# Kernel optimization log

Hardware: AMD Instinct MI355X
Metric: run time of the kernel (lower is better)

Reference implementation:

```python
import jax, jax.numpy as jnp
import numpy as np

B = 512            # graphs in batch
N = 246            # ROIs per graph per node type (Brainnetome atlas)
D = 256            # node feature dim (in_channels)
DEG = 32           # edges per node per edge type
RATIO = 0.8
K = int(np.ceil(RATIO * N))   # 197 nodes kept per graph (PyG topk uses ceil)
NT = B * N                    # total nodes per node type
E = B * N * DEG               # total edges per edge type
SLOPE = 0.2                   # HANConv leaky_relu negative slope


def _seg_softmax(logits, seg, num_segments):
    # numerically stable softmax over edges grouped by destination node
    m = jax.ops.segment_max(logits, seg, num_segments=num_segments)
    m = jnp.where(jnp.isfinite(m), m, 0.0)
    e = jnp.exp(logits - m[seg])
    s = jax.ops.segment_sum(e, seg, num_segments=num_segments)
    return e / (s[seg] + 1e-16)


def _edge_type_out(h_src, h_dst, ei, a_src, a_dst, n_dst):
    # one HANConv metapath: GAT-style attention + sum-aggregate + relu
    row, col = ei[0], ei[1]
    logit = jax.nn.leaky_relu((h_src * a_src).sum(-1)[row] + (h_dst * a_dst).sum(-1)[col], SLOPE)
    alpha = _seg_softmax(logit, col, n_dst)
    out = jax.ops.segment_sum(h_src[row] * alpha[:, None], col, num_segments=n_dst)
    return jax.nn.relu(out)


def _group(o1, o2, k_w, k_b, q):
    # HANConv semantic attention over the 2 metapaths hitting a node type
    stk = jnp.stack([o1, o2])                    # [2, NT, 1]
    t = jnp.tanh(stk @ k_w + k_b).mean(axis=1)   # [2, 1]
    w = jax.nn.softmax((q * t).sum(-1))          # [2]
    return (w[:, None, None] * stk).sum(0)       # [NT, 1]


def _han_scores(x_bold, x_dti, pw_b, pb_b, pw_d, pb_d, att, k_w, k_b, q, ei_bb, ei_bd, ei_db, ei_dd):
    h_b = x_bold @ pw_b + pb_b   # [NT, 1]
    h_d = x_dti @ pw_d + pb_d
    o_bb = _edge_type_out(h_b, h_b, ei_bb, att[0, 0], att[0, 1], NT)  # dst bold
    o_bd = _edge_type_out(h_b, h_d, ei_bd, att[1, 0], att[1, 1], NT)  # dst dti
    o_db = _edge_type_out(h_d, h_b, ei_db, att[2, 0], att[2, 1], NT)  # dst bold
    o_dd = _edge_type_out(h_d, h_d, ei_dd, att[3, 0], att[3, 1], NT)  # dst dti
    s_bold = _group(o_bb, o_db, k_w, k_b, q)[:, 0]
    s_dti = _group(o_bd, o_dd, k_w, k_b, q)[:, 0]
    return s_bold, s_dti


def _topk(score):
    # per-graph top-K (all graphs have exactly N nodes -> static K)
    _, idx = jax.lax.top_k(score.reshape(B, N), K)
    return (idx + (jnp.arange(B, dtype=idx.dtype) * N)[:, None]).reshape(-1)


def _mask_of(perm, num_nodes):
    return jnp.full((num_nodes,), -1, dtype=jnp.int32).at[perm].set(
        jnp.arange(perm.shape[0], dtype=jnp.int32))


def _filter(ei, mask_row, mask_col):
    # jit-compatible variant of filter_adj: keep full edge length, mark
    # dropped edges with -1 and return the validity mask (no compaction).
    r, c = mask_row[ei[0]], mask_col[ei[1]]
    valid = (r >= 0) & (c >= 0)
    return jnp.stack([jnp.where(valid, r, -1), jnp.where(valid, c, -1)]), valid


def setup_inputs() -> dict:
    key = jax.random.key(0)
    ks = jax.random.split(key, 12)

    def edges(k):
        k1, k2 = jax.random.split(k)
        base = jnp.repeat(jnp.arange(B, dtype=jnp.int32) * N, N * DEG)
        row = base + jax.random.randint(k1, (E,), 0, N, dtype=jnp.int32)
        col = base + jax.random.randint(k2, (E,), 0, N, dtype=jnp.int32)
        return jnp.stack([row, col])

    batch = jnp.repeat(jnp.arange(B, dtype=jnp.int32), N)
    return {
        "x_bold": jax.random.normal(ks[0], (NT, D), jnp.float32),
        "x_dti": jax.random.normal(ks[1], (NT, D), jnp.float32),
        "proj_w_bold": jax.random.normal(ks[2], (D, 1), jnp.float32) / np.float32(np.sqrt(D)),
        "proj_b_bold": jnp.zeros((1,), jnp.float32),
        "proj_w_dti": jax.random.normal(ks[3], (D, 1), jnp.float32) / np.float32(np.sqrt(D)),
        "proj_b_dti": jnp.zeros((1,), jnp.float32),
        "att": jax.random.normal(ks[4], (4, 2, 1), jnp.float32),
        "k_lin_w": jax.random.normal(ks[5], (1, 1), jnp.float32),
        "k_lin_b": jnp.zeros((1,), jnp.float32),
        "q": jax.random.normal(ks[6], (1,), jnp.float32),
        "ei_bb": edges(ks[7]),
        "ei_bd": edges(ks[8]),
        "ei_db": edges(ks[9]),
        "ei_dd": edges(ks[10]),
        "batch_bold": batch,
        "batch_dti": batch,
    }


def reference(x_bold, x_dti, proj_w_bold, proj_b_bold, proj_w_dti, proj_b_dti,
              att, k_lin_w, k_lin_b, q, ei_bb, ei_bd, ei_db, ei_dd,
              batch_bold, batch_dti):
    s_bold, s_dti = _han_scores(x_bold, x_dti, proj_w_bold, proj_b_bold,
                                proj_w_dti, proj_b_dti, att, k_lin_w, k_lin_b, q,
                                ei_bb, ei_bd, ei_db, ei_dd)
    perm_b = _topk(s_bold)
    perm_d = _topk(s_dti)
    xb = x_bold[perm_b] * jnp.tanh(s_bold[perm_b])[:, None]
    xd = x_dti[perm_d] * jnp.tanh(s_dti[perm_d])[:, None]
    mb = _mask_of(perm_b, NT)
    md = _mask_of(perm_d, NT)
    bb_f, v_bb = _filter(ei_bb, mb, mb)   # filter_adj_single on bold-bold
    dd_f, v_dd = _filter(ei_dd, md, md)   # filter_adj_single on dti-dti
    bd_f, v_bd = _filter(ei_bd, mb, md)   # filter_adj_multi mode=1
    db_f, v_db = _filter(ei_db, md, mb)   # filter_adj_multi mode=2
    return (xb, xd, bb_f, v_bb, bd_f, v_bd, db_f, v_db, dd_f, v_dd,
            batch_bold[perm_b], batch_dti[perm_d], perm_b, perm_d, s_bold, s_dti)
```

## Files before the change

kernel.cpp:

```cpp
#include <hip/hip_runtime.h>
#include <cmath>

#define BB   512
#define NN   246
#define DD   256
#define DEGC 32
#define KK   197
#define NTOT (BB*NN)
#define EE   (BB*NN*DEGC)
#define EPG  (NN*DEGC)
#define EPG4 (EPG/4)
#define BKK  (BB*KK)

#define O_XB     0LL
#define O_XD     25821184LL
#define O_E0     51642368LL
#define STRIDE3E 12091392LL
#define O_BATCHB 100007936LL
#define O_BATCHD 100108800LL
#define O_PERMB  100209664LL
#define O_PERMD  100310528LL
#define O_SB     100411392LL
#define O_SD     100537344LL

typedef float vf4 __attribute__((ext_vector_type(4)));
typedef int   vi4 __attribute__((ext_vector_type(4)));

__device__ __forceinline__ vi4 nt_load_i4(const int* p) {
    return __builtin_nontemporal_load((const vi4*)p);
}
__device__ __forceinline__ vf4 nt_load_f4(const float* p) {
    return __builtin_nontemporal_load((const vf4*)p);
}
__device__ __forceinline__ void nt_store_f4(float* p, vf4 v) {
    __builtin_nontemporal_store(v, (vf4*)p);
}
__device__ __forceinline__ void nt_store_f(float* p, float v) {
    __builtin_nontemporal_store(v, p);
}

__global__ __launch_bounds__(256) void proj_kernel(
    const float* __restrict__ xb, const float* __restrict__ xd,
    const float* __restrict__ wb, const float* __restrict__ bbp,
    const float* __restrict__ wd, const float* __restrict__ bdp,
    float* __restrict__ hb, float* __restrict__ hd,
    double* __restrict__ sums) {
    if (blockIdx.x == 0 && threadIdx.x < 4) sums[threadIdx.x] = 0.0;
    int wid  = (blockIdx.x * 256 + threadIdx.x) >> 6;
    int lane = threadIdx.x & 63;
    if (wid >= 2 * NTOT) return;
    const float* x; const float* w; const float* bp; float* h; int node;
    if (wid < NTOT) { x = xb; w = wb; bp = bbp; h = hb; node = wid; }
    else            { x = xd; w = wd; bp = bdp; h = hd; node = wid - NTOT; }
    vf4 xv = nt_load_f4(x + (long long)node * DD + 4 * lane);
    vf4 wv = *(const vf4*)(w + 4 * lane);
    double acc = (double)xv.x * wv.x + (double)xv.y * wv.y +
                 (double)xv.z * wv.z + (double)xv.w * wv.w;
#pragma unroll
    for (int m = 32; m; m >>= 1) acc += __shfl_xor(acc, m, 64);
    if (lane == 0) h[node] = __fadd_rn((float)acc, bp[0]);
}

__global__ __launch_bounds__(512) void att_kernel(
    const int* __restrict__ ei_bb, const int* __restrict__ ei_bd,
    const int* __restrict__ ei_db, const int* __restrict__ ei_dd,
    const float* __restrict__ hb, const float* __restrict__ hd,
    const float* __restrict__ att, const float* __restrict__ kwp,
    const float* __restrict__ kbp, float* __restrict__ o,
    double* __restrict__ sums) {
    __shared__ float hs_sh[NN];
    __shared__ float hd_sh[NN];
    __shared__ float s_sh[NN];
    __shared__ float num_sh[NN];
    __shared__ double part[8];

    int bid = blockIdx.x;
    int t   = bid >> 9;
    int g   = bid & 511;
    const int* ei = (t == 0) ? ei_bb : (t == 1) ? ei_bd : (t == 2) ? ei_db : ei_dd;
    const float* hs  = (t >= 2) ? hd : hb;
    const float* hdt = (t & 1)  ? hd : hb;
    float a_src = att[2 * t], a_dst = att[2 * t + 1];
    int base = g * NN;
    int tid  = threadIdx.x;

    if (tid < NN) {
        hs_sh[tid]  = hs[base + tid];
        hd_sh[tid]  = hdt[base + tid];
        s_sh[tid]   = 1e-16f;
        num_sh[tid] = 0.f;
    }
    __syncthreads();

    const int* rows = ei + g * EPG;
    const int* cols = ei + EE + g * EPG;

    for (int q = tid; q < EPG4; q += 512) {
        vi4 r4 = nt_load_i4(rows + 4 * q);
        vi4 c4 = nt_load_i4(cols + 4 * q);
#pragma unroll
        for (int j = 0; j < 4; ++j) {
            int r = r4[j] - base;
            int c = c4[j] - base;
            float hr = hs_sh[r];
            float l  = __fadd_rn(__fmul_rn(a_src, hr), __fmul_rn(a_dst, hd_sh[c]));
            l = (l >= 0.f) ? l : __fmul_rn(0.2f, l);
            float e = expf(l);
            atomicAdd(&s_sh[c], e);
            atomicAdd(&num_sh[c], __fmul_rn(hr, e));
        }
    }
    __syncthreads();

    float kw = kwp[0], kb = kbp[0];
    float my = 0.f;
    if (tid < NN) {
        float v = num_sh[tid] / s_sh[tid];
        v = (v > 0.f) ? v : 0.f;
        o[(long long)t * NTOT + base + tid] = v;
        my = tanhf(__fadd_rn(__fmul_rn(v, kw), kb));
    }
    double acc = (double)my;
#pragma unroll
    for (int m = 32; m; m >>= 1) acc += __shfl_xor(acc, m, 64);
    int lane = tid & 63, wv = tid >> 6;
    if (lane == 0) part[wv] = acc;
    __syncthreads();
    if (tid == 0) {
        double tot = 0.0;
#pragma unroll
        for (int i = 0; i < 8; ++i) tot += part[i];
        atomicAdd(&sums[t], tot);
    }
}

__global__ __launch_bounds__(256) void score_kernel(
    const float* __restrict__ o, const double* __restrict__ sums,
    const float* __restrict__ qp,
    float* __restrict__ sb, float* __restrict__ sd,
    float* __restrict__ osb, float* __restrict__ osd) {
    int i = blockIdx.x * 256 + threadIdx.x;
    float q = qp[0];
    float t0 = (float)(sums[0] / (double)NTOT);
    float t1 = (float)(sums[1] / (double)NTOT);
    float t2 = (float)(sums[2] / (double)NTOT);
    float t3 = (float)(sums[3] / (double)NTOT);
    float l0 = __fmul_rn(q, t0), l1 = __fmul_rn(q, t2);
    float mx = fmaxf(l0, l1);
    float e0 = expf(l0 - mx), e1 = expf(l1 - mx);
    float se = __fadd_rn(e0, e1);
    float w0 = e0 / se, w1 = e1 / se;
    float l2 = __fmul_rn(q, t1), l3 = __fmul_rn(q, t3);
    float mx2 = fmaxf(l2, l3);
    float e2 = expf(l2 - mx2), e3 = expf(l3 - mx2);
    float se2 = __fadd_rn(e2, e3);
    float w2 = e2 / se2, w3 = e3 / se2;
    float vb = __fadd_rn(__fmul_rn(w0, o[i]),        __fmul_rn(w1, o[2LL * NTOT + i]));
    float vd = __fadd_rn(__fmul_rn(w2, o[NTOT + i]), __fmul_rn(w3, o[3LL * NTOT + i]));
    sb[i] = vb; sd[i] = vd;
    nt_store_f(osb + i, vb); nt_store_f(osd + i, vd);
}

__global__ __launch_bounds__(256) void topk_kernel(
    const float* __restrict__ sb, const float* __restrict__ sd,
    const int* __restrict__ batch_b, const int* __restrict__ batch_d,
    int* __restrict__ mask_b, int* __restrict__ mask_d,
    int* __restrict__ perm_b, int* __restrict__ perm_d,
    float* __restrict__ out) {
    __shared__ float v[NN];
    int g = blockIdx.x & 511, which = blockIdx.x >> 9, tid = threadIdx.x;
    const float* s     = which ? sd : sb;
    const int*   batch = which ? batch_d : batch_b;
    int* mask  = which ? mask_d : mask_b;
    int* permi = which ? perm_d : perm_b;
    float* operm  = out + (which ? O_PERMD : O_PERMB);
    float* obatch = out + (which ? O_BATCHD : O_BATCHB);
    if (tid < NN) v[tid] = s[g * NN + tid];
    __syncthreads();
    if (tid < NN) {
        float mv = v[tid];
        int rank = 0;
#pragma unroll 4
        for (int j = 0; j < NN; ++j) {
            float vj = v[j];
            rank += (vj > mv) || (vj == mv && j < tid);
        }
        int gnode = g * NN + tid;
        if (rank < KK) {
            int gp = g * KK + rank;
            permi[gp] = gnode;
            nt_store_f(operm + gp, (float)gnode);
            nt_store_f(obatch + gp, (float)batch[gnode]);
            mask[gnode] = gp;
        } else {
            mask[gnode] = -1;
        }
    }
}

__global__ __launch_bounds__(256) void gather_kernel(
    const float* __restrict__ xb, const float* __restrict__ xd,
    const int* __restrict__ perm_b, const int* __restrict__ perm_d,
    const float* __restrict__ sb, const float* __restrict__ sd,
    float* __restrict__ out) {
    int wid  = (blockIdx.x * 256 + threadIdx.x) >> 6;
    int lane = threadIdx.x & 63;
    if (wid >= 2 * BKK) return;
    int which = wid >= BKK;
    int j = which ? wid - BKK : wid;
    const float* x    = which ? xd : xb;
    const int*   perm = which ? perm_d : perm_b;
    const float* s    = which ? sd : sb;
    long long obase   = which ? O_XD : O_XB;
    int p = perm[j];
    float scale = tanhf(s[p]);
    vf4 vv = nt_load_f4(x + (long long)p * DD + 4 * lane);
    vf4 r;
    r.x = vv.x * scale; r.y = vv.y * scale;
    r.z = vv.z * scale; r.w = vv.w * scale;
    nt_store_f4(out + obase + (long long)j * DD + 4 * lane, r);
}

__global__ __launch_bounds__(256) void filter_kernel(
    const int* __restrict__ ei_bb, const int* __restrict__ ei_bd,
    const int* __restrict__ ei_db, const int* __restrict__ ei_dd,
    const int* __restrict__ mask_b, const int* __restrict__ mask_d,
    float* __restrict__ out) {
    const int QE = EE / 4;
    int tid = blockIdx.x * 256 + threadIdx.x;
    if (tid >= 4 * QE) return;
    int t = tid / QE;
    int q = tid - t * QE;
    const int* ei = (t == 0) ? ei_bb : (t == 1) ? ei_bd : (t == 2) ? ei_db : ei_dd;
    const int* mr = (t >= 2) ? mask_d : mask_b;
    const int* mc = (t & 1)  ? mask_d : mask_b;
    vi4 r4 = nt_load_i4(ei + 4 * q);
    vi4 c4 = nt_load_i4(ei + EE + 4 * q);
    vf4 orow, ocol, oval;
#pragma unroll
    for (int j = 0; j < 4; ++j) {
        int r = mr[r4[j]];
        int c = mc[c4[j]];
        bool val = (r >= 0) && (c >= 0);
        orow[j] = val ? (float)r : -1.f;
        ocol[j] = val ? (float)c : -1.f;
        oval[j] = val ? 1.f : 0.f;
    }
    float* base = out + O_E0 + (long long)t * STRIDE3E;
    nt_store_f4(base + 4 * q,              orow);
    nt_store_f4(base + EE + 4 * q,         ocol);
    nt_store_f4(base + 2LL * EE + 4 * q,   oval);
}

extern "C" void kernel_launch(void* const* d_in, const int* in_sizes, int n_in,
                              void* d_out, int out_size, void* d_ws, size_t ws_size,
                              hipStream_t stream) {
    const float* x_bold = (const float*)d_in[0];
    const float* x_dti  = (const float*)d_in[1];
    const float* pw_b   = (const float*)d_in[2];
    const float* pb_b   = (const float*)d_in[3];
    const float* pw_d   = (const float*)d_in[4];
    const float* pb_d   = (const float*)d_in[5];
    const float* att    = (const float*)d_in[6];
    const float* k_w    = (const float*)d_in[7];
    const float* k_b    = (const float*)d_in[8];
    const float* qv     = (const float*)d_in[9];
    const int* ei_bb    = (const int*)d_in[10];
    const int* ei_bd    = (const int*)d_in[11];
    const int* ei_db    = (const int*)d_in[12];
    const int* ei_dd    = (const int*)d_in[13];
    const int* batch_b  = (const int*)d_in[14];
    const int* batch_d  = (const int*)d_in[15];
    float* out = (float*)d_out;

    char* w = (char*)d_ws;
    double* sums  = (double*)w;
    float*  hb    = (float*)(w + 64);
    float*  hd    = hb + NTOT;
    float*  obuf  = hd + NTOT;
    float*  sb    = obuf + 4LL * NTOT;
    float*  sd    = sb + NTOT;
    int* mask_b   = (int*)(sd + NTOT);
    int* mask_d   = mask_b + NTOT;
    int* perm_b   = mask_d + NTOT;
    int* perm_d   = perm_b + BKK;

    proj_kernel<<<2 * NTOT / 4, 256, 0, stream>>>(x_bold, x_dti, pw_b, pb_b,
                                                  pw_d, pb_d, hb, hd, sums);
    att_kernel<<<4 * BB, 512, 0, stream>>>(ei_bb, ei_bd, ei_db, ei_dd,
                                           hb, hd, att, k_w, k_b, obuf, sums);
    score_kernel<<<NTOT / 256, 256, 0, stream>>>(obuf, sums, qv, sb, sd,
                                                 out + O_SB, out + O_SD);
    topk_kernel<<<2 * BB, 256, 0, stream>>>(sb, sd, batch_b, batch_d,
                                            mask_b, mask_d, perm_b, perm_d, out);
    gather_kernel<<<2 * BKK * 64 / 256, 256, 0, stream>>>(x_bold, x_dti,
                                                          perm_b, perm_d,
                                                          sb, sd, out);
    filter_kernel<<<EE / 256, 256, 0, stream>>>(ei_bb, ei_bd, ei_db, ei_dd,
                                                mask_b, mask_d, out);
}
```

Measured before the change: 880.8 us.

## Fuse score into topk, merge gather and filter, replicate LDS atomics

Score combination now happens inside the per-graph top-k kernel, and the feature gather and edge filter share one launch. The filter reads per-graph masks from LDS instead of doing random global lookups. The attention kernel spreads its shared-memory atomics over four replicas to reduce contention and uses fast __expf. This removes two launches and the sb/sd round trip, at the cost of slightly different float summation order and exp precision.

```diff
diff --git a/kernel.cpp b/kernel.cpp
--- a/kernel.cpp
+++ b/kernel.cpp
@@ -22,6 +22,9 @@
 #define O_PERMD  100310528LL
 #define O_SB     100411392LL
 #define O_SD     100537344LL
+
+#define GATH_BLOCKS (2*BKK/8)
+#define FILT_BLOCKS (4*BB)
 
 typedef float vf4 __attribute__((ext_vector_type(4)));
 typedef int   vi4 __attribute__((ext_vector_type(4)));
@@ -70,8 +73,8 @@
     double* __restrict__ sums) {
     __shared__ float hs_sh[NN];
     __shared__ float hd_sh[NN];
-    __shared__ float s_sh[NN];
-    __shared__ float num_sh[NN];
+    __shared__ float s_sh[4][NN];
+    __shared__ float num_sh[4][NN];
     __shared__ double part[8];
 
     int bid = blockIdx.x;
@@ -87,13 +90,16 @@
     if (tid < NN) {
         hs_sh[tid]  = hs[base + tid];
         hd_sh[tid]  = hdt[base + tid];
-        s_sh[tid]   = 1e-16f;
-        num_sh[tid] = 0.f;
+        s_sh[0][tid] = 1e-16f; s_sh[1][tid] = 0.f;
+        s_sh[2][tid] = 0.f;    s_sh[3][tid] = 0.f;
+        num_sh[0][tid] = 0.f;  num_sh[1][tid] = 0.f;
+        num_sh[2][tid] = 0.f;  num_sh[3][tid] = 0.f;
     }
     __syncthreads();
 
     const int* rows = ei + g * EPG;
     const int* cols = ei + EE + g * EPG;
+    int rep = tid & 3;
 
     for (int q = tid; q < EPG4; q += 512) {
         vi4 r4 = nt_load_i4(rows + 4 * q);
@@ -105,9 +111,9 @@
             float hr = hs_sh[r];
             float l  = __fadd_rn(__fmul_rn(a_src, hr), __fmul_rn(a_dst, hd_sh[c]));
             l = (l >= 0.f) ? l : __fmul_rn(0.2f, l);
-            float e = expf(l);
-            atomicAdd(&s_sh[c], e);
-            atomicAdd(&num_sh[c], __fmul_rn(hr, e));
+            float e = __expf(l);
+            atomicAdd(&s_sh[rep][c], e);
+            atomicAdd(&num_sh[rep][c], __fmul_rn(hr, e));
         }
     }
     __syncthreads();
@@ -115,7 +121,9 @@
     float kw = kwp[0], kb = kbp[0];
     float my = 0.f;
     if (tid < NN) {
-        float v = num_sh[tid] / s_sh[tid];
+        float s = ((s_sh[0][tid] + s_sh[1][tid]) + (s_sh[2][tid] + s_sh[3][tid]));
+        float n = ((num_sh[0][tid] + num_sh[1][tid]) + (num_sh[2][tid] + num_sh[3][tid]));
+        float v = n / s;
         v = (v > 0.f) ? v : 0.f;
         o[(long long)t * NTOT + base + tid] = v;
         my = tanhf(__fadd_rn(__fmul_rn(v, kw), kb));
@@ -134,48 +142,49 @@
     }
 }
 
-__global__ __launch_bounds__(256) void score_kernel(
+__global__ __launch_bounds__(256) void score_topk_kernel(
     const float* __restrict__ o, const double* __restrict__ sums,
     const float* __restrict__ qp,
-    float* __restrict__ sb, float* __restrict__ sd,
-    float* __restrict__ osb, float* __restrict__ osd) {
-    int i = blockIdx.x * 256 + threadIdx.x;
-    float q = qp[0];
-    float t0 = (float)(sums[0] / (double)NTOT);
-    float t1 = (float)(sums[1] / (double)NTOT);
-    float t2 = (float)(sums[2] / (double)NTOT);
-    float t3 = (float)(sums[3] / (double)NTOT);
-    float l0 = __fmul_rn(q, t0), l1 = __fmul_rn(q, t2);
-    float mx = fmaxf(l0, l1);
-    float e0 = expf(l0 - mx), e1 = expf(l1 - mx);
-    float se = __fadd_rn(e0, e1);
-    float w0 = e0 / se, w1 = e1 / se;
-    float l2 = __fmul_rn(q, t1), l3 = __fmul_rn(q, t3);
-    float mx2 = fmaxf(l2, l3);
-    float e2 = expf(l2 - mx2), e3 = expf(l3 - mx2);
-    float se2 = __fadd_rn(e2, e3);
-    float w2 = e2 / se2, w3 = e3 / se2;
-    float vb = __fadd_rn(__fmul_rn(w0, o[i]),        __fmul_rn(w1, o[2LL * NTOT + i]));
-    float vd = __fadd_rn(__fmul_rn(w2, o[NTOT + i]), __fmul_rn(w3, o[3LL * NTOT + i]));
-    sb[i] = vb; sd[i] = vd;
-    nt_store_f(osb + i, vb); nt_store_f(osd + i, vd);
-}
-
-__global__ __launch_bounds__(256) void topk_kernel(
-    const float* __restrict__ sb, const float* __restrict__ sd,
     const int* __restrict__ batch_b, const int* __restrict__ batch_d,
     int* __restrict__ mask_b, int* __restrict__ mask_d,
     int* __restrict__ perm_b, int* __restrict__ perm_d,
     float* __restrict__ out) {
     __shared__ float v[NN];
     int g = blockIdx.x & 511, which = blockIdx.x >> 9, tid = threadIdx.x;
-    const float* s     = which ? sd : sb;
-    const int*   batch = which ? batch_d : batch_b;
+    float q = qp[0];
+    float t0 = (float)(sums[0] / (double)NTOT);
+    float t1 = (float)(sums[1] / (double)NTOT);
+    float t2 = (float)(sums[2] / (double)NTOT);
+    float t3 = (float)(sums[3] / (double)NTOT);
+    float wA, wB;
+    if (!which) {
+        float l0 = __fmul_rn(q, t0), l1 = __fmul_rn(q, t2);
+        float mx = fmaxf(l0, l1);
+        float e0 = expf(l0 - mx), e1 = expf(l1 - mx);
+        float se = __fadd_rn(e0, e1);
+        wA = e0 / se; wB = e1 / se;
+    } else {
+        float l0 = __fmul_rn(q, t1), l1 = __fmul_rn(q, t3);
+        float mx = fmaxf(l0, l1);
+        float e0 = expf(l0 - mx), e1 = expf(l1 - mx);
+        float se = __fadd_rn(e0, e1);
+        wA = e0 / se; wB = e1 / se;
+    }
+    const int* batch = which ? batch_d : batch_b;
     int* mask  = which ? mask_d : mask_b;
     int* permi = which ? perm_d : perm_b;
     float* operm  = out + (which ? O_PERMD : O_PERMB);
     float* obatch = out + (which ? O_BATCHD : O_BATCHB);
-    if (tid < NN) v[tid] = s[g * NN + tid];
+    float* oscore = out + (which ? O_SD : O_SB);
+
+    if (tid < NN) {
+        int i = g * NN + tid;
+        float oA = which ? o[NTOT + i] : o[i];
+        float oB = which ? o[3LL * NTOT + i] : o[2LL * NTOT + i];
+        float val = __fadd_rn(__fmul_rn(wA, oA), __fmul_rn(wB, oB));
+        v[tid] = val;
+        nt_store_f(oscore + i, val);
+    }
     __syncthreads();
     if (tid < NN) {
         float mv = v[tid];
@@ -198,58 +207,66 @@
     }
 }
 
-__global__ __launch_bounds__(256) void gather_kernel(
+__global__ __launch_bounds__(512) void epilogue_kernel(
     const float* __restrict__ xb, const float* __restrict__ xd,
     const int* __restrict__ perm_b, const int* __restrict__ perm_d,
-    const float* __restrict__ sb, const float* __restrict__ sd,
-    float* __restrict__ out) {
-    int wid  = (blockIdx.x * 256 + threadIdx.x) >> 6;
-    int lane = threadIdx.x & 63;
-    if (wid >= 2 * BKK) return;
-    int which = wid >= BKK;
-    int j = which ? wid - BKK : wid;
-    const float* x    = which ? xd : xb;
-    const int*   perm = which ? perm_d : perm_b;
-    const float* s    = which ? sd : sb;
-    long long obase   = which ? O_XD : O_XB;
-    int p = perm[j];
-    float scale = tanhf(s[p]);
-    vf4 vv = nt_load_f4(x + (long long)p * DD + 4 * lane);
-    vf4 r;
-    r.x = vv.x * scale; r.y = vv.y * scale;
-    r.z = vv.z * scale; r.w = vv.w * scale;
-    nt_store_f4(out + obase + (long long)j * DD + 4 * lane, r);
-}
-
-__global__ __launch_bounds__(256) void filter_kernel(
     const int* __restrict__ ei_bb, const int* __restrict__ ei_bd,
     const int* __restrict__ ei_db, const int* __restrict__ ei_dd,
     const int* __restrict__ mask_b, const int* __restrict__ mask_d,
     float* __restrict__ out) {
-    const int QE = EE / 4;
-    int tid = blockIdx.x * 256 + threadIdx.x;
-    if (tid >= 4 * QE) return;
-    int t = tid / QE;
-    int q = tid - t * QE;
-    const int* ei = (t == 0) ? ei_bb : (t == 1) ? ei_bd : (t == 2) ? ei_db : ei_dd;
-    const int* mr = (t >= 2) ? mask_d : mask_b;
-    const int* mc = (t & 1)  ? mask_d : mask_b;
-    vi4 r4 = nt_load_i4(ei + 4 * q);
-    vi4 c4 = nt_load_i4(ei + EE + 4 * q);
-    vf4 orow, ocol, oval;
-#pragma unroll
-    for (int j = 0; j < 4; ++j) {
-        int r = mr[r4[j]];
-        int c = mc[c4[j]];
-        bool val = (r >= 0) && (c >= 0);
-        orow[j] = val ? (float)r : -1.f;
-        ocol[j] = val ? (float)c : -1.f;
-        oval[j] = val ? 1.f : 0.f;
-    }
-    float* base = out + O_E0 + (long long)t * STRIDE3E;
-    nt_store_f4(base + 4 * q,              orow);
-    nt_store_f4(base + EE + 4 * q,         ocol);
-    nt_store_f4(base + 2LL * EE + 4 * q,   oval);
+    int b = blockIdx.x, tid = threadIdx.x;
+    if (b < GATH_BLOCKS) {
+        int wid  = (b * 512 + tid) >> 6;
+        int lane = tid & 63;
+        int which = wid >= BKK;
+        int j = which ? wid - BKK : wid;
+        const float* x    = which ? xd : xb;
+        const int*   perm = which ? perm_d : perm_b;
+        const float* s    = out + (which ? O_SD : O_SB);
+        long long obase   = which ? O_XD : O_XB;
+        int p = perm[j];
+        float scale = tanhf(s[p]);
+        vf4 vv = nt_load_f4(x + (long long)p * DD + 4 * lane);
+        vf4 r;
+        r.x = vv.x * scale; r.y = vv.y * scale;
+        r.z = vv.z * scale; r.w = vv.w * scale;
+        nt_store_f4(out + obase + (long long)j * DD + 4 * lane, r);
+    } else {
+        __shared__ int mr_sh[NN];
+        __shared__ int mc_sh[NN];
+        int fb = b - GATH_BLOCKS;
+        int t  = fb >> 9;
+        int g  = fb & 511;
+        const int* ei = (t == 0) ? ei_bb : (t == 1) ? ei_bd : (t == 2) ? ei_db : ei_dd;
+        const int* mr = (t >= 2) ? mask_d : mask_b;
+        const int* mc = (t & 1)  ? mask_d : mask_b;
+        int base = g * NN;
+        if (tid < NN) {
+            mr_sh[tid] = mr[base + tid];
+            mc_sh[tid] = mc[base + tid];
+        }
+        __syncthreads();
+        const int* rows = ei + g * EPG;
+        const int* cols = ei + EE + g * EPG;
+        float* obase = out + O_E0 + (long long)t * STRIDE3E + g * EPG;
+        for (int q = tid; q < EPG4; q += 512) {
+            vi4 r4 = nt_load_i4(rows + 4 * q);
+            vi4 c4 = nt_load_i4(cols + 4 * q);
+            vf4 orow, ocol, oval;
+#pragma unroll
+            for (int j = 0; j < 4; ++j) {
+                int r = mr_sh[r4[j] - base];
+                int c = mc_sh[c4[j] - base];
+                bool val = (r >= 0) && (c >= 0);
+                orow[j] = val ? (float)r : -1.f;
+                ocol[j] = val ? (float)c : -1.f;
+                oval[j] = val ? 1.f : 0.f;
+            }
+            nt_store_f4(obase + 4 * q,            orow);
+            nt_store_f4(obase + EE + 4 * q,       ocol);
+            nt_store_f4(obase + 2LL * EE + 4 * q, oval);
+        }
+    }
 }
 
 extern "C" void kernel_launch(void* const* d_in, const int* in_sizes, int n_in,
@@ -278,9 +295,7 @@
     float*  hb    = (float*)(w + 64);
     float*  hd    = hb + NTOT;
     float*  obuf  = hd + NTOT;
-    float*  sb    = obuf + 4LL * NTOT;
-    float*  sd    = sb + NTOT;
-    int* mask_b   = (int*)(sd + NTOT);
+    int* mask_b   = (int*)(obuf + 4LL * NTOT);
     int* mask_d   = mask_b + NTOT;
     int* perm_b   = mask_d + NTOT;
     int* perm_d   = perm_b + BKK;
@@ -289,13 +304,11 @@
                                                   pw_d, pb_d, hb, hd, sums);
     att_kernel<<<4 * BB, 512, 0, stream>>>(ei_bb, ei_bd, ei_db, ei_dd,
                                            hb, hd, att, k_w, k_b, obuf, sums);
-    score_kernel<<<NTOT / 256, 256, 0, stream>>>(obuf, sums, qv, sb, sd,
-                                                 out + O_SB, out + O_SD);
-    topk_kernel<<<2 * BB, 256, 0, stream>>>(sb, sd, batch_b, batch_d,
-                                            mask_b, mask_d, perm_b, perm_d, out);
-    gather_kernel<<<2 * BKK * 64 / 256, 256, 0, stream>>>(x_bold, x_dti,
-                                                          perm_b, perm_d,
-                                                          sb, sd, out);
-    filter_kernel<<<EE / 256, 256, 0, stream>>>(ei_bb, ei_bd, ei_db, ei_dd,
-                                                mask_b, mask_d, out);
-}
+    score_topk_kernel<<<2 * BB, 256, 0, stream>>>(obuf, sums, qv,
+                                                  batch_b, batch_d,
+                                                  mask_b, mask_d,
+                                                  perm_b, perm_d, out);
+    epilogue_kernel<<<GATH_BLOCKS + FILT_BLOCKS, 512, 0, stream>>>(
+        x_bold, x_dti, perm_b, perm_d,
+        ei_bb, ei_bd, ei_db, ei_dd, mask_b, mask_d, out);
+}
```

Measured after the change: 876.8 us. About the same (-0.5%).
